# Kernel tuning notes

Measured on AMD Instinct MI355X. Metric: run time of the kernel, lower is better.

Reference implementation:

```python
import jax, jax.numpy as jnp
import numpy as np

N_WIN = 8  # matches init kwarg n_win

def setup_inputs() -> dict:
    key = jax.random.key(0)
    k1, k2, k3 = jax.random.split(key, 3)
    c = 64
    x = jax.random.normal(k1, (1, c, 256, 256), dtype=jnp.float32)
    W = jax.random.normal(k2, (3 * c, c), dtype=jnp.float32) * 0.05
    bias = jax.random.normal(k3, (3 * c,), dtype=jnp.float32) * 0.05
    return {"x": x, "W": W, "bias": bias}

def reference(x, W, bias):
    b, c, h, w = x.shape
    n_h = n_w = N_WIN
    hs, ws = h // n_h, w // n_w
    nw = n_h * n_w
    # unfold into non-overlapping windows: [1, nw, hs*ws, c]
    xw = x.reshape(b, c, n_h, hs, n_w, ws)
    xw = xw.transpose(0, 2, 4, 3, 5, 1).reshape(1, nw, hs * ws, c)
    # shared QKV linear
    qkv = xw @ W.T + bias
    q, k, v = qkv[..., :c], qkv[..., c:2 * c], qkv[..., 2 * c:3 * c]
    # region-level routing via mean-pooled tokens
    q_r = q.mean(axis=2)  # [1, nw, c]
    k_r = k.mean(axis=2)
    a_r = jax.nn.relu(jnp.einsum('bic,bjc->bij', q_r, k_r))  # [1, nw, nw]
    # mix windows: a_r @ flattened(k/q) == window-mixing einsum
    k_m = jnp.einsum('bij,bjtc->bitc', a_r, k)
    q_m = jnp.einsum('bij,bjtc->bitc', a_r, q)
    # relu-gated windowed attention
    attn = jax.nn.relu(jnp.einsum('bitc,bisc->bits', q_m, k_m))  # [1, nw, T, T]
    o = jnp.einsum('bits,bisc->bitc', attn, v)  # [1, nw, T, c]
    # fold back to image
    o = o.reshape(b, n_h, n_w, hs, ws, c).transpose(0, 5, 1, 3, 2, 4).reshape(b, c, h, w)
    return o
```

## Files before the change

kernel.cpp:

```cpp
#include <hip/hip_runtime.h>

typedef _Float16 half_t;
typedef __attribute__((ext_vector_type(8))) _Float16 half8;
typedef __attribute__((ext_vector_type(4))) _Float16 half4;
typedef __attribute__((ext_vector_type(4))) float floatx4;
typedef __attribute__((ext_vector_type(16))) float floatx16;

#define MFMA16(A, B, C) __builtin_amdgcn_mfma_f32_16x16x32_f16((A), (B), (C), 0, 0, 0)
#define MFMA32(A, B, C) __builtin_amdgcn_mfma_f32_32x32x16_f16((A), (B), (C), 0, 0, 0)

__global__ __launch_bounds__(256) void k_qkv(
    const float* __restrict__ x, const float* __restrict__ W,
    const float* __restrict__ bias, half_t* __restrict__ q,
    half_t* __restrict__ k, half_t* __restrict__ vT,
    float* __restrict__ qp, float* __restrict__ kp) {
  __shared__ __align__(16) half_t Xs[128][72];
  __shared__ __align__(16) half_t Ws[192][72];
  __shared__ float qs_l[64], ks_l[64];
  const int w = blockIdx.y;
  const int tx = blockIdx.x;
  const int t0 = tx * 128;
  const int ih = w >> 3, iw = w & 7;
  const int xbase = ih * 8192 + iw * 32;
  const int tid = threadIdx.x;

  for (int i = tid; i < 8192; i += 256) {
    const int c = i >> 7, tt = i & 127;
    const int t = t0 + tt;
    Xs[tt][c] = (half_t)x[c * 65536 + xbase + (t >> 5) * 256 + (t & 31)];
  }
  for (int i = tid; i < 3072; i += 256) {
    const int o = i >> 4, c4 = (i & 15) * 4;
    const floatx4 v = *(const floatx4*)&W[o * 64 + c4];
    half4 hv;
    #pragma unroll
    for (int p = 0; p < 4; p++) hv[p] = (half_t)v[p];
    *(half4*)&Ws[o][c4] = hv;
  }
  if (tid < 64) { qs_l[tid] = 0.f; ks_l[tid] = 0.f; }
  __syncthreads();

  const int wave = tid >> 6, lane = tid & 63;
  const int lrow = lane & 15, lq = lane >> 4;
  const int rbase = (wave >> 1) * 64;
  const int cbase = (wave & 1) * 96;

  floatx4 acc[4][6];
  const floatx4 z = {0.f, 0.f, 0.f, 0.f};
  #pragma unroll
  for (int mt = 0; mt < 4; mt++)
    #pragma unroll
    for (int nt = 0; nt < 6; nt++) acc[mt][nt] = z;

  #pragma unroll
  for (int kf = 0; kf < 2; kf++) {
    const int koff = kf * 32 + lq * 8;
    half8 a[4], b[6];
    #pragma unroll
    for (int mt = 0; mt < 4; mt++)
      a[mt] = *(const half8*)&Xs[rbase + mt * 16 + lrow][koff];
    #pragma unroll
    for (int nt = 0; nt < 6; nt++)
      b[nt] = *(const half8*)&Ws[cbase + nt * 16 + lrow][koff];
    #pragma unroll
    for (int mt = 0; mt < 4; mt++)
      #pragma unroll
      for (int nt = 0; nt < 6; nt++)
        acc[mt][nt] = MFMA16(a[mt], b[nt], acc[mt][nt]);
  }

  #pragma unroll
  for (int nt = 0; nt < 6; nt++) {
    const int o = cbase + nt * 16 + lrow;
    const float bs = bias[o];
    if (o < 64) {
      float s = 0.f;
      #pragma unroll
      for (int mt = 0; mt < 4; mt++) {
        const int tr = t0 + rbase + mt * 16 + lq * 4;
        #pragma unroll
        for (int r = 0; r < 4; r++) {
          const float v = acc[mt][nt][r] + bs;
          q[w * 65536 + (tr + r) * 64 + o] = (half_t)v;
          s += v;
        }
      }
      atomicAdd(&qs_l[o], s);
    } else if (o < 128) {
      const int oc = o - 64;
      float s = 0.f;
      #pragma unroll
      for (int mt = 0; mt < 4; mt++) {
        const int tr = t0 + rbase + mt * 16 + lq * 4;
        #pragma unroll
        for (int r = 0; r < 4; r++) {
          const float v = acc[mt][nt][r] + bs;
          k[w * 65536 + (tr + r) * 64 + oc] = (half_t)v;
          s += v;
        }
      }
      atomicAdd(&ks_l[oc], s);
    } else {
      const int oc = o - 128;
      #pragma unroll
      for (int mt = 0; mt < 4; mt++) {
        const int tr = t0 + rbase + mt * 16 + lq * 4;
        half4 pk;
        #pragma unroll
        for (int r = 0; r < 4; r++) pk[r] = (half_t)(acc[mt][nt][r] + bs);
        *(half4*)&vT[w * 65536 + oc * 1024 + tr] = pk;
      }
    }
  }
  __syncthreads();
  if (tid < 64) {
    qp[(w * 8 + tx) * 64 + tid] = qs_l[tid];
    kp[(w * 8 + tx) * 64 + tid] = ks_l[tid];
  }
}

__global__ __launch_bounds__(256) void k_ar(const float* __restrict__ qp,
                                            const float* __restrict__ kp,
                                            half_t* __restrict__ arH) {
  __shared__ float qs[64][65];
  __shared__ float ks[64][65];
  const int tid = threadIdx.x;
  for (int e = tid; e < 4096; e += 256) {
    const int i = e >> 6, c = e & 63;
    float sq = 0.f, sk = 0.f;
    #pragma unroll
    for (int t = 0; t < 8; t++) {
      sq += qp[i * 512 + t * 64 + c];
      sk += kp[i * 512 + t * 64 + c];
    }
    qs[i][c] = sq;
    ks[i][c] = sk;
  }
  __syncthreads();
  const float scale = 1.f / (1024.f * 1024.f);
  const int e = blockIdx.x * 256 + tid;
  const int i = e >> 6, j = e & 63;
  float s = 0.f;
  #pragma unroll
  for (int c = 0; c < 64; c++) s += qs[i][c] * ks[j][c];
  s *= scale;
  arH[e] = (half_t)(s > 0.f ? s : 0.f);
}

__global__ __launch_bounds__(256) void k_mix(const half_t* __restrict__ q,
                                             const half_t* __restrict__ k,
                                             const half_t* __restrict__ arH,
                                             half_t* __restrict__ qm,
                                             half_t* __restrict__ km) {
  const half_t* __restrict__ src = blockIdx.y ? k : q;
  half_t* __restrict__ dst = blockIdx.y ? km : qm;
  const int tid = threadIdx.x;
  const int wave = tid >> 6, lane = tid & 63;
  const int ln31 = lane & 31;
  const int hk8 = (lane >> 5) * 8;

  half8 aA[2][4];
  #pragma unroll
  for (int mt = 0; mt < 2; mt++)
    #pragma unroll
    for (int kk = 0; kk < 4; kk++)
      aA[mt][kk] = *(const half8*)&arH[(mt * 32 + ln31) * 64 + kk * 16 + hk8];

  #pragma unroll
  for (int t32 = 0; t32 < 2; t32++) {
    const int pos = blockIdx.x * 256 + wave * 64 + t32 * 32 + ln31;
    half8 bB[4];
    #pragma unroll
    for (int kk = 0; kk < 4; kk++)
      #pragma unroll
      for (int jj = 0; jj < 8; jj++)
        bB[kk][jj] = src[(kk * 16 + hk8 + jj) * 65536 + pos];

    floatx16 c0, c1;
    #pragma unroll
    for (int r = 0; r < 16; r++) { c0[r] = 0.f; c1[r] = 0.f; }
    #pragma unroll
    for (int kk = 0; kk < 4; kk++) {
      c0 = MFMA32(aA[0][kk], bB[kk], c0);
      c1 = MFMA32(aA[1][kk], bB[kk], c1);
    }
    const int h4 = (lane >> 5) * 4;
    #pragma unroll
    for (int r = 0; r < 16; r++) {
      const int row = (r & 3) + h4 + 8 * (r >> 2);
      dst[row * 65536 + pos] = (half_t)c0[r];
      dst[(32 + row) * 65536 + pos] = (half_t)c1[r];
    }
  }
}

__global__ __launch_bounds__(256, 2) void k_attn(const half_t* __restrict__ qm,
                                                 const half_t* __restrict__ km,
                                                 const half_t* __restrict__ vT,
                                                 float* __restrict__ out) {
  __shared__ __align__(16) char smem[70656];
  half_t (*Ks)[72]  = (half_t (*)[72])(smem);
  half_t (*Vs)[136] = (half_t (*)[136])(smem + 18432);
  half_t (*St)[136] = (half_t (*)[136])(smem + 35840);
  float (*Of)[132]  = (float (*)[132])(smem);

  const int w = blockIdx.y;
  const int t0 = blockIdx.x * 128;
  const int tid = threadIdx.x;
  const int wave = tid >> 6, lane = tid & 63;
  const int ln31 = lane & 31;
  const int hk8 = (lane >> 5) * 8, hk4 = (lane >> 5) * 4;
  const int w32 = wave * 32;
  const int wbase = w * 65536;

  half8 bQ[4][4];
  #pragma unroll
  for (int tt = 0; tt < 4; tt++)
    #pragma unroll
    for (int kk = 0; kk < 4; kk++)
      bQ[tt][kk] = *(const half8*)&qm[wbase + (t0 + tt * 32 + ln31) * 64 + kk * 16 + hk8];

  floatx16 oacc[2];
  #pragma unroll
  for (int ct = 0; ct < 2; ct++)
    #pragma unroll
    for (int r = 0; r < 16; r++) oacc[ct][r] = 0.f;

  for (int sc = 0; sc < 8; sc++) {
    const int s0 = sc * 128;
    __syncthreads();
    for (int idx = tid; idx < 1024; idx += 256) {
      const int r = idx >> 3, co = (idx & 7) * 8;
      *(half8*)&Ks[r][co] = *(const half8*)&km[wbase + (s0 + r) * 64 + co];
    }
    for (int idx = tid; idx < 1024; idx += 256) {
      const int c = idx >> 4, so = (idx & 15) * 8;
      *(half8*)&Vs[c][so] = *(const half8*)&vT[wbase + c * 1024 + s0 + so];
    }
    __syncthreads();

    floatx16 sacc[4];
    #pragma unroll
    for (int tt = 0; tt < 4; tt++)
      #pragma unroll
      for (int r = 0; r < 16; r++) sacc[tt][r] = 0.f;
    half8 aK[4];
    #pragma unroll
    for (int kk = 0; kk < 4; kk++)
      aK[kk] = *(const half8*)&Ks[w32 + ln31][kk * 16 + hk8];
    #pragma unroll
    for (int kk = 0; kk < 4; kk++)
      #pragma unroll
      for (int tt = 0; tt < 4; tt++)
        sacc[tt] = MFMA32(aK[kk], bQ[tt][kk], sacc[tt]);

    #pragma unroll
    for (int tt = 0; tt < 4; tt++) {
      const int t = tt * 32 + ln31;
      #pragma unroll
      for (int g = 0; g < 4; g++) {
        const int s = w32 + g * 8 + hk4;
        half4 pk;
        #pragma unroll
        for (int p = 0; p < 4; p++) {
          const float v = sacc[tt][g * 4 + p];
          pk[p] = (half_t)(v > 0.f ? v : 0.f);
        }
        *(half4*)&St[t][s] = pk;
      }
    }
    __syncthreads();

    #pragma unroll
    for (int kk = 0; kk < 8; kk++) {
      const half8 aS = *(const half8*)&St[w32 + ln31][kk * 16 + hk8];
      #pragma unroll
      for (int ct = 0; ct < 2; ct++) {
        const half8 bV = *(const half8*)&Vs[ct * 32 + ln31][kk * 16 + hk8];
        oacc[ct] = MFMA32(aS, bV, oacc[ct]);
      }
    }
  }
  __syncthreads();
  #pragma unroll
  for (int ct = 0; ct < 2; ct++) {
    const int c = ct * 32 + ln31;
    #pragma unroll
    for (int g = 0; g < 4; g++) {
      const int tl = w32 + g * 8 + hk4;
      floatx4 f;
      #pragma unroll
      for (int p = 0; p < 4; p++) f[p] = oacc[ct][g * 4 + p];
      *(floatx4*)&Of[c][tl] = f;
    }
  }
  __syncthreads();
  const int ih = w >> 3, iw = w & 7;
  const int obase = ih * 8192 + iw * 32;
  for (int i = tid; i < 2048; i += 256) {
    const int c = i >> 5, tq = (i & 31) * 4;
    const int t = t0 + tq;
    *(floatx4*)&out[c * 65536 + obase + (t >> 5) * 256 + (t & 31)] =
        *(const floatx4*)&Of[c][tq];
  }
}

extern "C" void kernel_launch(void* const* d_in, const int* in_sizes, int n_in,
                              void* d_out, int out_size, void* d_ws, size_t ws_size,
                              hipStream_t stream) {
  const float* x = (const float*)d_in[0];
  const float* W = (const float*)d_in[1];
  const float* bias = (const float*)d_in[2];
  float* out = (float*)d_out;

  half_t* q = (half_t*)d_ws;
  half_t* k = q + 4194304;
  half_t* vT = k + 4194304;
  half_t* qm = vT + 4194304;
  half_t* km = qm + 4194304;
  float* qp = (float*)(km + 4194304);
  float* kp = qp + 32768;
  half_t* arH = (half_t*)(kp + 32768);

  k_qkv<<<dim3(8, 64), 256, 0, stream>>>(x, W, bias, q, k, vT, qp, kp);
  k_ar<<<16, 256, 0, stream>>>(qp, kp, arH);
  k_mix<<<dim3(256, 2), 256, 0, stream>>>(q, k, arH, qm, km);
  k_attn<<<dim3(8, 64), 256, 0, stream>>>(qm, km, vT, out);
}
```

Before: 132.3 us.

## Load K fragments directly from global and write output straight from accumulators

The attention kernel no longer stages K tiles in shared memory. Each wave now loads its K fragments directly from global memory into registers. The PV MFMA operands are swapped so the accumulator is laid out as channel-by-token, which lets results go straight to the output without a shared-memory transpose and the two barriers around it. The St stride is also padded to 138 to cut bank conflicts. These changes reduce LDS footprint and traffic, which may raise occupancy, but the output stores are now scalar 4-byte writes rather than float4 vectors.

```diff
diff --git a/kernel.cpp b/kernel.cpp
--- a/kernel.cpp
+++ b/kernel.cpp
@@ -198,12 +198,8 @@
                                                  const half_t* __restrict__ km,
                                                  const half_t* __restrict__ vT,
                                                  float* __restrict__ out) {
-  __shared__ __align__(16) char smem[70656];
-  half_t (*Ks)[72]  = (half_t (*)[72])(smem);
-  half_t (*Vs)[136] = (half_t (*)[136])(smem + 18432);
-  half_t (*St)[136] = (half_t (*)[136])(smem + 35840);
-  float (*Of)[132]  = (float (*)[132])(smem);
-
+  __shared__ __align__(16) half_t Vs[64][136];
+  __shared__ __align__(16) half_t St[128][138];
   const int w = blockIdx.y;
   const int t0 = blockIdx.x * 128;
   const int tid = threadIdx.x;
@@ -230,13 +226,13 @@
     const int s0 = sc * 128;
     __syncthreads();
     for (int idx = tid; idx < 1024; idx += 256) {
-      const int r = idx >> 3, co = (idx & 7) * 8;
-      *(half8*)&Ks[r][co] = *(const half8*)&km[wbase + (s0 + r) * 64 + co];
-    }
-    for (int idx = tid; idx < 1024; idx += 256) {
       const int c = idx >> 4, so = (idx & 15) * 8;
       *(half8*)&Vs[c][so] = *(const half8*)&vT[wbase + c * 1024 + s0 + so];
     }
+    half8 aK[4];
+    #pragma unroll
+    for (int kk = 0; kk < 4; kk++)
+      aK[kk] = *(const half8*)&km[wbase + (s0 + w32 + ln31) * 64 + kk * 16 + hk8];
     __syncthreads();
 
     floatx16 sacc[4];
@@ -244,10 +240,6 @@
     for (int tt = 0; tt < 4; tt++)
       #pragma unroll
       for (int r = 0; r < 16; r++) sacc[tt][r] = 0.f;
-    half8 aK[4];
-    #pragma unroll
-    for (int kk = 0; kk < 4; kk++)
-      aK[kk] = *(const half8*)&Ks[w32 + ln31][kk * 16 + hk8];
     #pragma unroll
     for (int kk = 0; kk < 4; kk++)
       #pragma unroll
@@ -273,35 +265,26 @@
 
     #pragma unroll
     for (int kk = 0; kk < 8; kk++) {
-      const half8 aS = *(const half8*)&St[w32 + ln31][kk * 16 + hk8];
+      const half8 bS = *(const half8*)&St[w32 + ln31][kk * 16 + hk8];
       #pragma unroll
       for (int ct = 0; ct < 2; ct++) {
-        const half8 bV = *(const half8*)&Vs[ct * 32 + ln31][kk * 16 + hk8];
-        oacc[ct] = MFMA32(aS, bV, oacc[ct]);
-      }
-    }
-  }
-  __syncthreads();
-  #pragma unroll
-  for (int ct = 0; ct < 2; ct++) {
-    const int c = ct * 32 + ln31;
-    #pragma unroll
-    for (int g = 0; g < 4; g++) {
-      const int tl = w32 + g * 8 + hk4;
-      floatx4 f;
-      #pragma unroll
-      for (int p = 0; p < 4; p++) f[p] = oacc[ct][g * 4 + p];
-      *(floatx4*)&Of[c][tl] = f;
-    }
-  }
-  __syncthreads();
+        const half8 aV = *(const half8*)&Vs[ct * 32 + ln31][kk * 16 + hk8];
+        oacc[ct] = MFMA32(aV, bS, oacc[ct]);
+      }
+    }
+  }
+
   const int ih = w >> 3, iw = w & 7;
   const int obase = ih * 8192 + iw * 32;
-  for (int i = tid; i < 2048; i += 256) {
-    const int c = i >> 5, tq = (i & 31) * 4;
-    const int t = t0 + tq;
-    *(floatx4*)&out[c * 65536 + obase + (t >> 5) * 256 + (t & 31)] =
-        *(const floatx4*)&Of[c][tq];
+  const int tb = ((t0 + w32) >> 5) * 256 + ln31;
+  const int h4 = (lane >> 5) * 4;
+  #pragma unroll
+  for (int ct = 0; ct < 2; ct++) {
+    #pragma unroll
+    for (int r = 0; r < 16; r++) {
+      const int c = ct * 32 + (r & 3) + h4 + 8 * (r >> 2);
+      out[c * 65536 + obase + tb] = oacc[ct][r];
+    }
   }
 }
 
```

Measured after the change: 129.4 us. 2.2% less time.
